# Performance work log

Measured on AMD Instinct MI355X. Metric: run time of the kernel, lower is better.

## Reference

```python
import jax, jax.numpy as jnp
import numpy as np

EPS = 1e-5  # torch BatchNorm1d default eps

N_NODES = 100000
N_EDGES = 1250000
N_GRAPHS = 512
F_IN = 16
HID = 64


def _bn(x, w, b):
    # track_running_stats=False, momentum=None -> always batch statistics (biased var)
    m = jnp.mean(x, axis=0)
    v = jnp.var(x, axis=0)
    return (x - m) * jax.lax.rsqrt(v + EPS) * w + b


def _prelu(x, a):
    return jnp.where(x >= 0, x, a * x)


def _gcn_conv(x, W, b, src, dst, n):
    # PyG GCNConv: h = x W; add self loops; sym-norm by deg^-1/2 on target degrees
    h = x @ W  # [N, out]
    ones = jnp.ones(src.shape[0], x.dtype)
    deg = jax.ops.segment_sum(ones, dst, num_segments=n) + 1.0  # +1 self loop
    dis = jax.lax.rsqrt(deg)  # deg >= 1 so finite
    norm = (dis[src] * dis[dst])[:, None]  # [E,1]
    agg = jax.ops.segment_sum(h[src] * norm, dst, num_segments=n)
    # self-loop contribution: norm = dis[i]*dis[i]
    return agg + h * (dis * dis)[:, None] + b


def setup_inputs() -> dict:
    key = jax.random.key(0)
    ks = jax.random.split(key, 12)
    x = jax.random.normal(ks[0], (N_NODES, F_IN), dtype=jnp.float32)
    edge_index = jax.random.randint(ks[1], (2, N_EDGES), 0, N_NODES, dtype=jnp.int32)
    # evenly spaced graph ids so every segment is non-empty (global_max_pool)
    batch = ((jnp.arange(N_NODES, dtype=jnp.int32) * N_GRAPHS) // N_NODES).astype(jnp.int32)
    s = 0.1
    W1 = jax.random.normal(ks[2], (F_IN, HID), jnp.float32) * s
    b1 = jnp.zeros((HID,), jnp.float32)
    W2 = jax.random.normal(ks[3], (HID, HID), jnp.float32) * s
    b2 = jnp.zeros((HID,), jnp.float32)
    lw1 = jax.random.normal(ks[4], (HID, HID), jnp.float32) * s
    lb1 = jnp.zeros((HID,), jnp.float32)
    lw2 = jax.random.normal(ks[5], (HID, 1), jnp.float32) * s
    lb2 = jnp.zeros((1,), jnp.float32)
    bn1_w = jnp.ones((HID,), jnp.float32); bn1_b = jnp.zeros((HID,), jnp.float32)
    bn2_w = jnp.ones((HID,), jnp.float32); bn2_b = jnp.zeros((HID,), jnp.float32)
    bn3_w = jnp.ones((HID,), jnp.float32); bn3_b = jnp.zeros((HID,), jnp.float32)
    bn4_w = jnp.ones((1,), jnp.float32); bn4_b = jnp.zeros((1,), jnp.float32)
    a1 = jnp.full((1,), 0.25, jnp.float32)
    a2 = jnp.full((1,), 0.25, jnp.float32)
    a3 = jnp.full((1,), 0.25, jnp.float32)
    a4 = jnp.full((1,), 0.25, jnp.float32)
    return {"x": x, "edge_index": edge_index, "batch": batch,
            "W1": W1, "b1": b1, "W2": W2, "b2": b2,
            "bn1_w": bn1_w, "bn1_b": bn1_b, "bn2_w": bn2_w, "bn2_b": bn2_b,
            "bn3_w": bn3_w, "bn3_b": bn3_b, "bn4_w": bn4_w, "bn4_b": bn4_b,
            "lw1": lw1, "lb1": lb1, "lw2": lw2, "lb2": lb2,
            "a1": a1, "a2": a2, "a3": a3, "a4": a4}


def reference(x, edge_index, batch, W1, b1, W2, b2,
              bn1_w, bn1_b, bn2_w, bn2_b, bn3_w, bn3_b, bn4_w, bn4_b,
              lw1, lb1, lw2, lb2, a1, a2, a3, a4):
    src, dst = edge_index[0], edge_index[1]
    n = x.shape[0]
    h = _gcn_conv(x, W1, b1, src, dst, n)
    h = _prelu(_bn(h, bn1_w, bn1_b), a1)
    h = _gcn_conv(h, W2, b2, src, dst, n)
    h = _prelu(_bn(h, bn2_w, bn2_b), a2)
    g = jax.ops.segment_max(h, batch, num_segments=N_GRAPHS)  # global_max_pool
    g = _prelu(_bn(g @ lw1 + lb1, bn3_w, bn3_b), a3)
    g = _prelu(_bn(g @ lw2 + lb2, bn4_w, bn4_b), a4)
    return g
```

## Files before the change

### kernel.cpp

```cpp
#include <hip/hip_runtime.h>
#include <hip/hip_bf16.h>

#define N_NODES 100000
#define N_EDGES 1250000
#define N_GRAPHS 512
#define F_IN 16
#define HID 64
#define EPS 1e-5f

#define K_B 1563
#define B_H 250
#define EPB 5000
#define M_SC (K_B * B_H)
#define SC_BLKS ((M_SC + 1023) / 1024)

typedef unsigned int uint;

__device__ __forceinline__ uint f2bf(float f) {
    uint u = __float_as_uint(f);
    return (u + 0x7fffu + ((u >> 16) & 1u)) >> 16;
}
__device__ __forceinline__ uint pack2(float lo, float hi) {
    return f2bf(lo) | (f2bf(hi) << 16);
}
__device__ __forceinline__ void unpack8(float* o, uint4 v) {
    o[0] = __uint_as_float(v.x << 16); o[1] = __uint_as_float(v.x & 0xffff0000u);
    o[2] = __uint_as_float(v.y << 16); o[3] = __uint_as_float(v.y & 0xffff0000u);
    o[4] = __uint_as_float(v.z << 16); o[5] = __uint_as_float(v.z & 0xffff0000u);
    o[6] = __uint_as_float(v.w << 16); o[7] = __uint_as_float(v.w & 0xffff0000u);
}
__device__ __forceinline__ void accum8(float* a, uint4 v) {
    a[0] += __uint_as_float(v.x << 16); a[1] += __uint_as_float(v.x & 0xffff0000u);
    a[2] += __uint_as_float(v.y << 16); a[3] += __uint_as_float(v.y & 0xffff0000u);
    a[4] += __uint_as_float(v.z << 16); a[5] += __uint_as_float(v.z & 0xffff0000u);
    a[6] += __uint_as_float(v.w << 16); a[7] += __uint_as_float(v.w & 0xffff0000u);
}


__global__ __launch_bounds__(256) void k_hist(const int4* __restrict__ dst4,
                                              int* __restrict__ hist,
                                              float* __restrict__ statsr) {
    __shared__ int h[K_B];
    int t = threadIdx.x, b = blockIdx.x;
    if (b == 0) {
        for (int i = t; i < 6 * 512; i += 256) statsr[i] = 0.f;
    }
    for (int k = t; k < K_B; k += 256) h[k] = 0;
    __syncthreads();
    const int4* d4 = dst4 + b * (EPB / 4);
    for (int i = t; i < EPB / 4; i += 256) {
        int4 d = d4[i];
        atomicAdd(&h[d.x >> 6], 1);
        atomicAdd(&h[d.y >> 6], 1);
        atomicAdd(&h[d.z >> 6], 1);
        atomicAdd(&h[d.w >> 6], 1);
    }
    __syncthreads();
    for (int k = t; k < K_B; k += 256) hist[k * B_H + b] = h[k];
}

__global__ void k_s1(const int* __restrict__ in, int* __restrict__ out,
                     int* __restrict__ bsum, int n) {
    __shared__ int sh[256];
    int blk = blockIdx.x, t = threadIdx.x;
    int base = blk * 1024 + t * 4;
    int v[4];
#pragma unroll
    for (int j = 0; j < 4; j++) { int i = base + j; v[j] = (i < n) ? in[i] : 0; }
    int tsum = v[0] + v[1] + v[2] + v[3];
    sh[t] = tsum;
    __syncthreads();
    for (int ofs = 1; ofs < 256; ofs <<= 1) {
        int x = (t >= ofs) ? sh[t - ofs] : 0;
        __syncthreads();
        sh[t] += x;
        __syncthreads();
    }
    int run = sh[t] - tsum;
    if (t == 255) bsum[blk] = sh[255];
#pragma unroll
    for (int j = 0; j < 4; j++) { int i = base + j; if (i < n) out[i] = run; run += v[j]; }
}

__global__ __launch_bounds__(256) void k_bucketize(const int4* __restrict__ src4,
        const int4* __restrict__ dst4, const int* __restrict__ ebase,
        const int* __restrict__ bsum, int* __restrict__ ebuck) {
    __shared__ int base[K_B];
    __shared__ int bss[512];
    __shared__ int shs[256];
    int t = threadIdx.x, b = blockIdx.x;
    {
        int i0 = 2 * t, i1 = 2 * t + 1;
        int v0 = (i0 < SC_BLKS) ? bsum[i0] : 0;
        int v1 = (i1 < SC_BLKS) ? bsum[i1] : 0;
        int s = v0 + v1;
        shs[t] = s;
        __syncthreads();
        for (int ofs = 1; ofs < 256; ofs <<= 1) {
            int x2 = (t >= ofs) ? shs[t - ofs] : 0;
            __syncthreads();
            shs[t] += x2;
            __syncthreads();
        }
        int run = shs[t] - s;
        bss[i0] = run;
        bss[i1] = run + v0;
    }
    __syncthreads();
    for (int k = t; k < K_B; k += 256) {
        int idx = k * B_H + b;
        base[k] = ebase[idx] + bss[idx >> 10];
    }
    __syncthreads();
    const int4* s4 = src4 + b * (EPB / 4);
    const int4* d4 = dst4 + b * (EPB / 4);
    for (int i = t; i < EPB / 4; i += 256) {
        int s = s4[i].x, s_y = s4[i].y, s_z = s4[i].z, s_w = s4[i].w;
        int4 sv = s4[i];
        int4 d = d4[i];
        (void)s; (void)s_y; (void)s_z; (void)s_w;
        int p;
        p = atomicAdd(&base[d.x >> 6], 1); ebuck[p] = sv.x | ((d.x & 63) << 17);
        p = atomicAdd(&base[d.y >> 6], 1); ebuck[p] = sv.y | ((d.y & 63) << 17);
        p = atomicAdd(&base[d.z >> 6], 1); ebuck[p] = sv.z | ((d.z & 63) << 17);
        p = atomicAdd(&base[d.w >> 6], 1); ebuck[p] = sv.w | ((d.w & 63) << 17);
    }
}

__global__ __launch_bounds__(256) void k_csr(const int* __restrict__ ebase,
        const int* __restrict__ bsum, const int* __restrict__ ebuck,
        int* __restrict__ col, int2* __restrict__ meta, float* __restrict__ dis,
        const float* __restrict__ x, const float* __restrict__ W1,
        ushort* __restrict__ A) {
    int k = blockIdx.x, t = threadIdx.x;
    __shared__ int eb[2048];
    __shared__ int cnt512[512];
    __shared__ int off512[512];
    __shared__ int sb[512];
    __shared__ int sh[256];
    __shared__ int bss[512];
    __shared__ float Ws[F_IN * HID];
    __shared__ float xs2[64 * F_IN];
    __shared__ float disS[64];
    {
        int i0 = 2 * t, i1 = 2 * t + 1;
        int v0 = (i0 < SC_BLKS) ? bsum[i0] : 0;
        int v1 = (i1 < SC_BLKS) ? bsum[i1] : 0;
        int s = v0 + v1;
        sh[t] = s;
        __syncthreads();
        for (int ofs = 1; ofs < 256; ofs <<= 1) {
            int x2 = (t >= ofs) ? sh[t - ofs] : 0;
            __syncthreads();
            sh[t] += x2;
            __syncthreads();
        }
        int run = sh[t] - s;
        bss[i0] = run;
        bss[i1] = run + v0;
    }
    __syncthreads();
    int i0 = k * B_H;
    int beg = ebase[i0] + bss[i0 >> 10];
    int end;
    if (k + 1 < K_B) {
        int i1 = i0 + B_H;
        end = ebase[i1] + bss[i1 >> 10];
    } else {
        end = N_EDGES;
    }
    int m = end - beg;
    for (int i = t; i < F_IN * HID; i += 256) Ws[i] = W1[i];
    for (int i = t; i < 64 * F_IN; i += 256) {
        int gi = k * (64 * F_IN) + i;
        xs2[i] = (gi < N_NODES * F_IN) ? x[gi] : 0.f;
    }
    for (int i = t; i < 512; i += 256) cnt512[i] = 0;
    __syncthreads();
    if (m <= 2048) {
        for (int i = t; i < m; i += 256) {
            int e = ebuck[beg + i];
            eb[i] = e;
            int bin = ((e >> 17) << 3) | ((e & 0x1FFFF) >> 14);
            atomicAdd(&cnt512[bin], 1);
        }
        __syncthreads();
        int v0 = cnt512[2 * t], v1 = cnt512[2 * t + 1];
        int pair = v0 + v1;
        sh[t] = pair;
        __syncthreads();
        for (int ofs = 1; ofs < 256; ofs <<= 1) {
            int x2 = (t >= ofs) ? sh[t - ofs] : 0;
            __syncthreads();
            sh[t] += x2;
            __syncthreads();
        }
        int excl = sh[t] - pair;
        off512[2 * t] = excl;
        off512[2 * t + 1] = excl + v0;
        sb[2 * t] = beg + excl;
        sb[2 * t + 1] = beg + excl + v0;
        __syncthreads();
        if (t < 64) {
            int o0 = off512[t * 8];
            int o1 = (t < 63) ? off512[(t + 1) * 8] : m;
            int node = k * 64 + t;
            int deg = o1 - o0;
            float dv = rsqrtf((float)deg + 1.0f);
            disS[t] = dv;
            if (node < N_NODES) {
                meta[node] = make_int2(beg + o0, deg);
                dis[node] = dv;
            }
        }
        __syncthreads();
        for (int i = t; i < m; i += 256) {
            int e = eb[i];
            int bin = ((e >> 17) << 3) | ((e & 0x1FFFF) >> 14);
            int pos = atomicAdd(&sb[bin], 1);
            col[pos] = e & 0x1FFFF;
        }
    } else {
        for (int i = t; i < m; i += 256) atomicAdd(&cnt512[ebuck[beg + i] >> 17], 1);
        __syncthreads();
        if (t < 64) {
            int v = cnt512[t];
            int incl = v;
#pragma unroll
            for (int o = 1; o < 64; o <<= 1) { int u = __shfl_up(incl, o); if (t >= o) incl += u; }
            int excl = incl - v;
            int node = k * 64 + t;
            float dv = rsqrtf((float)v + 1.0f);
            disS[t] = dv;
            if (node < N_NODES) {
                meta[node] = make_int2(beg + excl, v);
                dis[node] = dv;
            }
            sb[t] = beg + excl;
        }
        __syncthreads();
        for (int i = t; i < m; i += 256) {
            int e = ebuck[beg + i];
            int pos = atomicAdd(&sb[e >> 17], 1);
            col[pos] = e & 0x1FFFF;
        }
    }
#pragma unroll
    for (int i = 0; i < 16; i++) {
        int idx = i * 256 + t;
        int n = idx >> 6, f = idx & 63;
        float acc = 0.f;
#pragma unroll
        for (int kk = 0; kk < F_IN; kk++)
            acc = fmaf(xs2[n * F_IN + kk], Ws[kk * HID + f], acc);
        int gn = k * 64 + n;
        if (gn < N_NODES)
            A[(size_t)gn * HID + f] = (ushort)f2bf(acc * disS[n]);
    }
}


__global__ __launch_bounds__(512) void k_gemm2(const ushort* __restrict__ B,
        const float* __restrict__ s1r, const float* __restrict__ ss1r,
        const float* __restrict__ bnw, const float* __restrict__ bnb,
        const float* __restrict__ alpha, const float* __restrict__ W2,
        const float* __restrict__ dis, ushort* __restrict__ A2) {
    __shared__ float Ws[HID * HID];
    __shared__ float xs[32 * HID];
    __shared__ float scs[64], shsv[64];
    int t = threadIdx.x;
#pragma unroll
    for (int i = 0; i < 8; i++) Ws[i * 512 + t] = W2[i * 512 + t];
    if (t < 64) {
        float s = 0, q = 0;
#pragma unroll
        for (int r = 0; r < 8; r++) { s += s1r[r * 64 + t]; q += ss1r[r * 64 + t]; }
        const float invn = 1.f / N_NODES;
        float m = s * invn;
        float v = q * invn - m * m;
        float sc = bnw[t] * rsqrtf(v + EPS);
        scs[t] = sc;
        shsv[t] = bnb[t] - m * sc;
    }
    __syncthreads();
    int n0 = blockIdx.x * 32;
    float al = alpha[0];
    {
        const uint* Bu = (const uint*)(B + (size_t)n0 * HID);
#pragma unroll
        for (int i = 0; i < 2; i++) {
            int idx = i * 512 + t;
            uint u = Bu[idx];
            int fp = (idx & 31) * 2;
            int row = idx >> 5;
            float lo = __uint_as_float(u << 16) * scs[fp] + shsv[fp];
            float hi = __uint_as_float(u & 0xffff0000u) * scs[fp + 1] + shsv[fp + 1];
            lo = lo >= 0.f ? lo : al * lo;
            hi = hi >= 0.f ? hi : al * hi;
            xs[row * HID + fp] = lo;
            xs[row * HID + fp + 1] = hi;
        }
    }
    __syncthreads();
    int f = t & 63, w = t >> 6;
    float Wreg[HID];
#pragma unroll
    for (int k = 0; k < HID; k++) Wreg[k] = Ws[k * HID + f];
#pragma unroll
    for (int i = 0; i < 4; i++) {
        int nl = w * 4 + i;
        float acc = 0.f;
#pragma unroll
        for (int kq = 0; kq < 16; kq++) {
            const float4 xv = *(const float4*)&xs[nl * HID + kq * 4];
            acc = fmaf(xv.x, Wreg[4 * kq + 0], acc);
            acc = fmaf(xv.y, Wreg[4 * kq + 1], acc);
            acc = fmaf(xv.z, Wreg[4 * kq + 2], acc);
            acc = fmaf(xv.w, Wreg[4 * kq + 3], acc);
        }
        int n = n0 + nl;
        A2[(size_t)n * HID + f] = (ushort)f2bf(acc * dis[n]);
    }
}

__global__ __launch_bounds__(256) void k_agg(const uint4* __restrict__ Asc,
        const float* __restrict__ dis, const int2* __restrict__ meta,
        const int* __restrict__ col, const float* __restrict__ bias,
        uint4* __restrict__ outB, float* __restrict__ sumr,
        float* __restrict__ sumsqr) {
    int t = threadIdx.x;
    int nid = blockIdx.x * 32 + (t >> 3);
    int fq = t & 7;
    int2 mt = meta[nid];
    int beg = mt.x, m = mt.y;
    float acc[8] = {0, 0, 0, 0, 0, 0, 0, 0};
    int j = 0;
    for (; j + 8 <= m; j += 8) {
        int s0 = col[beg + j];
        int s1 = col[beg + j + 1];
        int s2 = col[beg + j + 2];
        int s3 = col[beg + j + 3];
        int s4 = col[beg + j + 4];
        int s5 = col[beg + j + 5];
        int s6 = col[beg + j + 6];
        int s7 = col[beg + j + 7];
        uint4 r0 = Asc[(size_t)s0 * 8 + fq];
        uint4 r1 = Asc[(size_t)s1 * 8 + fq];
        uint4 r2 = Asc[(size_t)s2 * 8 + fq];
        uint4 r3 = Asc[(size_t)s3 * 8 + fq];
        uint4 r4 = Asc[(size_t)s4 * 8 + fq];
        uint4 r5 = Asc[(size_t)s5 * 8 + fq];
        uint4 r6 = Asc[(size_t)s6 * 8 + fq];
        uint4 r7 = Asc[(size_t)s7 * 8 + fq];
        accum8(acc, r0); accum8(acc, r1); accum8(acc, r2); accum8(acc, r3);
        accum8(acc, r4); accum8(acc, r5); accum8(acc, r6); accum8(acc, r7);
    }
    for (; j + 2 <= m; j += 2) {
        int s0 = col[beg + j];
        int s1 = col[beg + j + 1];
        uint4 r0 = Asc[(size_t)s0 * 8 + fq];
        uint4 r1 = Asc[(size_t)s1 * 8 + fq];
        accum8(acc, r0); accum8(acc, r1);
    }
    if (j < m) {
        int s = col[beg + j];
        accum8(acc, Asc[(size_t)s * 8 + fq]);
    }
    accum8(acc, Asc[(size_t)nid * 8 + fq]);
    float dn = dis[nid];
    float4 b0 = ((const float4*)bias)[fq * 2];
    float4 b1 = ((const float4*)bias)[fq * 2 + 1];
    float o[8];
    o[0] = b0.x + dn * acc[0]; o[1] = b0.y + dn * acc[1];
    o[2] = b0.z + dn * acc[2]; o[3] = b0.w + dn * acc[3];
    o[4] = b1.x + dn * acc[4]; o[5] = b1.y + dn * acc[5];
    o[6] = b1.z + dn * acc[6]; o[7] = b1.w + dn * acc[7];
    uint4 ov;
    ov.x = pack2(o[0], o[1]); ov.y = pack2(o[2], o[3]);
    ov.z = pack2(o[4], o[5]); ov.w = pack2(o[6], o[7]);
    outB[(size_t)nid * 8 + fq] = ov;

    float sq[8];
#pragma unroll
    for (int i = 0; i < 8; i++) sq[i] = o[i] * o[i];
#pragma unroll
    for (int ofs = 8; ofs <= 32; ofs <<= 1) {
#pragma unroll
        for (int i = 0; i < 8; i++) {
            o[i] += __shfl_xor(o[i], ofs);
            sq[i] += __shfl_xor(sq[i], ofs);
        }
    }
    __shared__ float ps[4][64], pq[4][64];
    int w = t >> 6, lane = t & 63;
    if (lane < 8) {
#pragma unroll
        for (int i = 0; i < 8; i++) {
            ps[w][lane * 8 + i] = o[i];
            pq[w][lane * 8 + i] = sq[i];
        }
    }
    __syncthreads();
    if (t < 64) {
        float a = ps[0][t] + ps[1][t] + ps[2][t] + ps[3][t];
        float b = pq[0][t] + pq[1][t] + pq[2][t] + pq[3][t];
        int rep = (blockIdx.x & 7) * 64;
        atomicAdd(&sumr[rep + t], a);
        atomicAdd(&sumsqr[rep + t], b);
    }
}

__global__ __launch_bounds__(256) void k_pool(const uint4* __restrict__ a,
        const float* __restrict__ s2r, const float* __restrict__ ss2r,
        const float* __restrict__ bnw, const float* __restrict__ bnb,
        const float* __restrict__ alpha, const float* __restrict__ lw1,
        const float* __restrict__ lb1, float* __restrict__ th,
        float* __restrict__ s3r, float* __restrict__ ss3r) {
    __shared__ float scs[64], shsv[64];
    __shared__ float sm[2048];
    __shared__ float gr[64];
    int gi = blockIdx.x;
    int t = threadIdx.x, rg = t >> 3, fq = t & 7;
    if (t < 64) {
        float s = 0, q = 0;
#pragma unroll
        for (int r = 0; r < 8; r++) { s += s2r[r * 64 + t]; q += ss2r[r * 64 + t]; }
        const float invn = 1.f / N_NODES;
        float m = s * invn;
        float v = q * invn - m * m;
        float sc = bnw[t] * rsqrtf(v + EPS);
        scs[t] = sc;
        shsv[t] = bnb[t] - m * sc;
    }
    __syncthreads();
    int lo = (gi * N_NODES + N_GRAPHS - 1) / N_GRAPHS;
    int hi = ((gi + 1) * N_NODES + N_GRAPHS - 1) / N_GRAPHS;
    float al = alpha[0];
    float sc[8], sh[8];
#pragma unroll
    for (int i = 0; i < 8; i++) { sc[i] = scs[fq * 8 + i]; sh[i] = shsv[fq * 8 + i]; }
    float mx[8];
#pragma unroll
    for (int i = 0; i < 8; i++) mx[i] = -INFINITY;
    for (int r = lo + rg; r < hi; r += 32) {
        float o[8];
        unpack8(o, a[(size_t)r * 8 + fq]);
#pragma unroll
        for (int i = 0; i < 8; i++) {
            float v = o[i] * sc[i] + sh[i];
            v = v >= 0.f ? v : al * v;
            mx[i] = fmaxf(mx[i], v);
        }
    }
#pragma unroll
    for (int i = 0; i < 8; i++) sm[rg * 64 + fq * 8 + i] = mx[i];
    __syncthreads();
    if (t < 64) {
        float m = sm[t];
#pragma unroll
        for (int i = 1; i < 32; i++) m = fmaxf(m, sm[i * 64 + t]);
        gr[t] = m;
    }
    __syncthreads();
    if (t < 64) {
        float acc = lb1[t];
#pragma unroll
        for (int k = 0; k < 64; k++) acc = fmaf(gr[k], lw1[k * 64 + t], acc);
        th[gi * 64 + t] = acc;
        int rep = (gi & 7) * 64;
        atomicAdd(&s3r[rep + t], acc);
        atomicAdd(&ss3r[rep + t], acc * acc);
    }
}

__global__ __launch_bounds__(512) void k_head(const float* __restrict__ th,
        const float* __restrict__ s3r, const float* __restrict__ ss3r,
        const float* __restrict__ bn3w, const float* __restrict__ bn3b,
        const float* __restrict__ a3, const float* __restrict__ lw2,
        const float* __restrict__ lb2, const float* __restrict__ bn4w,
        const float* __restrict__ bn4b, const float* __restrict__ a4,
        float* __restrict__ out) {
    int t = threadIdx.x, w = t >> 6, lane = t & 63;
    __shared__ float t2s[N_GRAPHS];
    __shared__ float rs[8], rq[8];
    const float invn = 1.f / N_GRAPHS;
    float s = 0, q = 0;
#pragma unroll
    for (int r = 0; r < 8; r++) { s += s3r[r * 64 + lane]; q += ss3r[r * 64 + lane]; }
    float m3 = s * invn;
    float v3 = q * invn - m3 * m3;
    float sc3 = bn3w[lane] * rsqrtf(v3 + EPS);
    float sh3 = bn3b[lane] - m3 * sc3;
    float al3 = a3[0];
    float wv = lw2[lane];
    float lb = lb2[0];
    for (int r = w; r < N_GRAPHS; r += 8) {
        float xv = th[r * 64 + lane] * sc3 + sh3;
        xv = xv >= 0.f ? xv : al3 * xv;
        float p = xv * wv;
#pragma unroll
        for (int o = 32; o > 0; o >>= 1) p += __shfl_xor(p, o);
        if (lane == 0) t2s[r] = p + lb;
    }
    __syncthreads();
    float tv = t2s[t];
    float ps = tv, pq = tv * tv;
#pragma unroll
    for (int o = 32; o > 0; o >>= 1) { ps += __shfl_xor(ps, o); pq += __shfl_xor(pq, o); }
    if (lane == 0) { rs[w] = ps; rq[w] = pq; }
    __syncthreads();
    float S = 0, Q = 0;
#pragma unroll
    for (int i = 0; i < 8; i++) { S += rs[i]; Q += rq[i]; }
    float m4 = S * invn;
    float v4 = Q * invn - m4 * m4;
    float sc4 = bn4w[0] * rsqrtf(v4 + EPS);
    float xb = (tv - m4) * sc4 + bn4b[0];
    float al4 = a4[0];
    out[t] = xb >= 0.f ? xb : al4 * xb;
}

extern "C" void kernel_launch(void* const* d_in, const int* in_sizes, int n_in,
                              void* d_out, int out_size, void* d_ws, size_t ws_size,
                              hipStream_t stream) {
    const float* x   = (const float*)d_in[0];
    const int*   ei  = (const int*)d_in[1];
    const int4*  src4 = (const int4*)ei;
    const int4*  dst4 = (const int4*)(ei + N_EDGES);
    const float* W1  = (const float*)d_in[3];
    const float* b1  = (const float*)d_in[4];
    const float* W2  = (const float*)d_in[5];
    const float* b2  = (const float*)d_in[6];
    const float* bn1w = (const float*)d_in[7];
    const float* bn1b = (const float*)d_in[8];
    const float* bn2w = (const float*)d_in[9];
    const float* bn2b = (const float*)d_in[10];
    const float* bn3w = (const float*)d_in[11];
    const float* bn3b = (const float*)d_in[12];
    const float* bn4w = (const float*)d_in[13];
    const float* bn4b = (const float*)d_in[14];
    const float* lw1  = (const float*)d_in[15];
    const float* lb1  = (const float*)d_in[16];
    const float* lw2  = (const float*)d_in[17];
    const float* lb2  = (const float*)d_in[18];
    const float* a1   = (const float*)d_in[19];
    const float* a2   = (const float*)d_in[20];
    const float* a3   = (const float*)d_in[21];
    const float* a4   = (const float*)d_in[22];
    float* out = (float*)d_out;

    char* p = (char*)d_ws;
    auto carve = [&](size_t bytes) -> void* {
        void* r = (void*)p;
        p += (bytes + 255) & ~(size_t)255;
        return r;
    };
    int*    hist = (int*)carve((size_t)M_SC * 4);
    int*    ebase = (int*)carve((size_t)M_SC * 4);
    int*    ebuck = (int*)carve((size_t)N_EDGES * 4);
    int*    col  = (int*)carve((size_t)N_EDGES * 4);
    float*  dis  = (float*)carve((size_t)N_NODES * 4);
    int2*   meta = (int2*)carve((size_t)N_NODES * 8);
    int*    bsum = (int*)carve(4096);
    ushort* A    = (ushort*)carve((size_t)N_NODES * HID * 2);
    ushort* B    = (ushort*)carve((size_t)N_NODES * HID * 2);
    float*  th   = (float*)carve((size_t)N_GRAPHS * HID * 4);
    float*  statsr = (float*)carve(6 * 512 * 4);
    float* s1r = statsr,          *ss1r = statsr + 512;
    float* s2r = statsr + 1024,   *ss2r = statsr + 1536;
    float* s3r = statsr + 2048,   *ss3r = statsr + 2560;

    k_hist<<<B_H, 256, 0, stream>>>(dst4, hist, statsr);
    k_s1<<<SC_BLKS, 256, 0, stream>>>(hist, ebase, bsum, M_SC);
    k_bucketize<<<B_H, 256, 0, stream>>>(src4, dst4, ebase, bsum, ebuck);
    k_csr<<<K_B, 256, 0, stream>>>(ebase, bsum, ebuck, col, meta, dis, x, W1, A);

    const int NB32 = N_NODES / 32;
    k_agg<<<NB32, 256, 0, stream>>>((const uint4*)A, dis, meta, col, b1, (uint4*)B,
                                    s1r, ss1r);
    k_gemm2<<<NB32, 512, 0, stream>>>(B, s1r, ss1r, bn1w, bn1b, a1, W2, dis, A);
    k_agg<<<NB32, 256, 0, stream>>>((const uint4*)A, dis, meta, col, b2, (uint4*)B,
                                    s2r, ss2r);
    k_pool<<<N_GRAPHS, 256, 0, stream>>>((const uint4*)B, s2r, ss2r, bn2w, bn2b, a2,
                                         lw1, lb1, th, s3r, ss3r);
    k_head<<<1, 512, 0, stream>>>(th, s3r, ss3r, bn3w, bn3b, a3, lw2, lb2,
                                  bn4w, bn4b, a4, out);
}
```

Baseline: 181.9 us.

## Sort nodes by degree within 64-node chunks to balance aggregation warps

k_csr now ranks the 64 nodes of each chunk by in-degree and writes a permutation, and k_agg processes nodes in that order so nodes of similar degree share a wavefront. This is meant to reduce divergence from uneven loop trip counts across the 8 nodes in a wave. In exchange it adds a perm lookup, padded slots with an inactive guard, slightly more blocks, and less locality in output writes.

```diff
diff --git a/kernel.cpp b/kernel.cpp
--- a/kernel.cpp
+++ b/kernel.cpp
@@ -13,6 +13,7 @@
 #define EPB 5000
 #define M_SC (K_B * B_H)
 #define SC_BLKS ((M_SC + 1023) / 1024)
+#define N_SLOTS (K_B * 64)
 
 typedef unsigned int uint;
 
@@ -115,10 +116,8 @@
     const int4* s4 = src4 + b * (EPB / 4);
     const int4* d4 = dst4 + b * (EPB / 4);
     for (int i = t; i < EPB / 4; i += 256) {
-        int s = s4[i].x, s_y = s4[i].y, s_z = s4[i].z, s_w = s4[i].w;
         int4 sv = s4[i];
         int4 d = d4[i];
-        (void)s; (void)s_y; (void)s_z; (void)s_w;
         int p;
         p = atomicAdd(&base[d.x >> 6], 1); ebuck[p] = sv.x | ((d.x & 63) << 17);
         p = atomicAdd(&base[d.y >> 6], 1); ebuck[p] = sv.y | ((d.y & 63) << 17);
@@ -130,6 +129,7 @@
 __global__ __launch_bounds__(256) void k_csr(const int* __restrict__ ebase,
         const int* __restrict__ bsum, const int* __restrict__ ebuck,
         int* __restrict__ col, int2* __restrict__ meta, float* __restrict__ dis,
+        int* __restrict__ perm,
         const float* __restrict__ x, const float* __restrict__ W1,
         ushort* __restrict__ A) {
     int k = blockIdx.x, t = threadIdx.x;
@@ -142,6 +142,7 @@
     __shared__ float Ws[F_IN * HID];
     __shared__ float xs2[64 * F_IN];
     __shared__ float disS[64];
+    __shared__ int degS[64];
     {
         int i0 = 2 * t, i1 = 2 * t + 1;
         int v0 = (i0 < SC_BLKS) ? bsum[i0] : 0;
@@ -208,6 +209,7 @@
             int deg = o1 - o0;
             float dv = rsqrtf((float)deg + 1.0f);
             disS[t] = dv;
+            degS[t] = deg;
             if (node < N_NODES) {
                 meta[node] = make_int2(beg + o0, deg);
                 dis[node] = dv;
@@ -232,6 +234,7 @@
             int node = k * 64 + t;
             float dv = rsqrtf((float)v + 1.0f);
             disS[t] = dv;
+            degS[t] = v;
             if (node < N_NODES) {
                 meta[node] = make_int2(beg + excl, v);
                 dis[node] = dv;
@@ -244,6 +247,16 @@
             int pos = atomicAdd(&sb[e >> 17], 1);
             col[pos] = e & 0x1FFFF;
         }
+    }
+    if (t < 64) {
+        int d = degS[t];
+        int rank = 0;
+#pragma unroll
+        for (int j = 0; j < 64; j++) {
+            int dj = degS[j];
+            rank += (dj < d) || (dj == d && j < t);
+        }
+        perm[k * 64 + rank] = k * 64 + t;
     }
 #pragma unroll
     for (int i = 0; i < 16; i++) {
@@ -325,14 +338,19 @@
 
 __global__ __launch_bounds__(256) void k_agg(const uint4* __restrict__ Asc,
         const float* __restrict__ dis, const int2* __restrict__ meta,
-        const int* __restrict__ col, const float* __restrict__ bias,
-        uint4* __restrict__ outB, float* __restrict__ sumr,
-        float* __restrict__ sumsqr) {
+        const int* __restrict__ col, const int* __restrict__ perm,
+        const float* __restrict__ bias, uint4* __restrict__ outB,
+        float* __restrict__ sumr, float* __restrict__ sumsqr) {
     int t = threadIdx.x;
-    int nid = blockIdx.x * 32 + (t >> 3);
+    int nid = perm[blockIdx.x * 32 + (t >> 3)];
     int fq = t & 7;
-    int2 mt = meta[nid];
-    int beg = mt.x, m = mt.y;
+    bool act = nid < N_NODES;
+    int beg = 0, m = 0; float dn = 0.f;
+    if (act) {
+        int2 mt = meta[nid];
+        beg = mt.x; m = mt.y;
+        dn = dis[nid];
+    }
     float acc[8] = {0, 0, 0, 0, 0, 0, 0, 0};
     int j = 0;
     for (; j + 8 <= m; j += 8) {
@@ -366,19 +384,23 @@
         int s = col[beg + j];
         accum8(acc, Asc[(size_t)s * 8 + fq]);
     }
-    accum8(acc, Asc[(size_t)nid * 8 + fq]);
-    float dn = dis[nid];
-    float4 b0 = ((const float4*)bias)[fq * 2];
-    float4 b1 = ((const float4*)bias)[fq * 2 + 1];
     float o[8];
-    o[0] = b0.x + dn * acc[0]; o[1] = b0.y + dn * acc[1];
-    o[2] = b0.z + dn * acc[2]; o[3] = b0.w + dn * acc[3];
-    o[4] = b1.x + dn * acc[4]; o[5] = b1.y + dn * acc[5];
-    o[6] = b1.z + dn * acc[6]; o[7] = b1.w + dn * acc[7];
-    uint4 ov;
-    ov.x = pack2(o[0], o[1]); ov.y = pack2(o[2], o[3]);
-    ov.z = pack2(o[4], o[5]); ov.w = pack2(o[6], o[7]);
-    outB[(size_t)nid * 8 + fq] = ov;
+    if (act) {
+        accum8(acc, Asc[(size_t)nid * 8 + fq]);
+        float4 b0 = ((const float4*)bias)[fq * 2];
+        float4 b1 = ((const float4*)bias)[fq * 2 + 1];
+        o[0] = b0.x + dn * acc[0]; o[1] = b0.y + dn * acc[1];
+        o[2] = b0.z + dn * acc[2]; o[3] = b0.w + dn * acc[3];
+        o[4] = b1.x + dn * acc[4]; o[5] = b1.y + dn * acc[5];
+        o[6] = b1.z + dn * acc[6]; o[7] = b1.w + dn * acc[7];
+        uint4 ov;
+        ov.x = pack2(o[0], o[1]); ov.y = pack2(o[2], o[3]);
+        ov.z = pack2(o[4], o[5]); ov.w = pack2(o[6], o[7]);
+        outB[(size_t)nid * 8 + fq] = ov;
+    } else {
+#pragma unroll
+        for (int i = 0; i < 8; i++) o[i] = 0.f;
+    }
 
     float sq[8];
 #pragma unroll
@@ -561,6 +583,7 @@
     int*    col  = (int*)carve((size_t)N_EDGES * 4);
     float*  dis  = (float*)carve((size_t)N_NODES * 4);
     int2*   meta = (int2*)carve((size_t)N_NODES * 8);
+    int*    perm = (int*)carve((size_t)N_SLOTS * 4);
     int*    bsum = (int*)carve(4096);
     ushort* A    = (ushort*)carve((size_t)N_NODES * HID * 2);
     ushort* B    = (ushort*)carve((size_t)N_NODES * HID * 2);
@@ -573,14 +596,15 @@
     k_hist<<<B_H, 256, 0, stream>>>(dst4, hist, statsr);
     k_s1<<<SC_BLKS, 256, 0, stream>>>(hist, ebase, bsum, M_SC);
     k_bucketize<<<B_H, 256, 0, stream>>>(src4, dst4, ebase, bsum, ebuck);
-    k_csr<<<K_B, 256, 0, stream>>>(ebase, bsum, ebuck, col, meta, dis, x, W1, A);
+    k_csr<<<K_B, 256, 0, stream>>>(ebase, bsum, ebuck, col, meta, dis, perm, x, W1, A);
 
     const int NB32 = N_NODES / 32;
-    k_agg<<<NB32, 256, 0, stream>>>((const uint4*)A, dis, meta, col, b1, (uint4*)B,
-                                    s1r, ss1r);
+    const int AGG_BLKS = N_SLOTS / 32;
+    k_agg<<<AGG_BLKS, 256, 0, stream>>>((const uint4*)A, dis, meta, col, perm, b1,
+                                        (uint4*)B, s1r, ss1r);
     k_gemm2<<<NB32, 512, 0, stream>>>(B, s1r, ss1r, bn1w, bn1b, a1, W2, dis, A);
-    k_agg<<<NB32, 256, 0, stream>>>((const uint4*)A, dis, meta, col, b2, (uint4*)B,
-                                    s2r, ss2r);
+    k_agg<<<AGG_BLKS, 256, 0, stream>>>((const uint4*)A, dis, meta, col, perm, b2,
+                                        (uint4*)B, s2r, ss2r);
     k_pool<<<N_GRAPHS, 256, 0, stream>>>((const uint4*)B, s2r, ss2r, bn2w, bn2b, a2,
                                          lw1, lb1, th, s3r, ss3r);
     k_head<<<1, 512, 0, stream>>>(th, s3r, ss3r, bn3w, bn3b, a3, lw2, lb2,
```

Result: slower. 190.2 us (+4.6%).
